# Optimization experiments

Measured on AMD Instinct MI355X. Metric: run time of the kernel, lower is better.

The kernel has to match this reference:

```python
import jax, jax.numpy as jnp
import numpy as np


def setup_inputs() -> dict:
    key = jax.random.key(0)
    ks = jax.random.split(key, 4)
    B, T, D, U = 32, 1024, 1024, 1024
    x = jax.random.normal(ks[0], (B, T, D), dtype=jnp.float32)
    W = jax.random.normal(ks[1], (D, 4 * U), dtype=jnp.float32) * (1.0 / np.sqrt(D))
    b = jnp.zeros((4 * U,), dtype=jnp.float32)
    Vr = jax.random.normal(ks[2], (U,), dtype=jnp.float32) * 0.1
    Vf = jax.random.normal(ks[3], (U,), dtype=jnp.float32) * 0.1
    h0 = jnp.zeros((B, U), dtype=jnp.float32)
    c0 = jnp.zeros((B, U), dtype=jnp.float32)
    return {"x": x, "h0": h0, "c0": c0, "W": W, "b": b, "Vr": Vr, "Vf": Vf}


def _sru(x, h0, c0, W, b, Vr, Vf):
    B, T, D = x.shape
    U = Vr.shape[0]
    # Batched matmul across all timesteps, then sequential elementwise scan.
    g = jnp.einsum('btd,dk->btk', x, W) + b            # [B, T, 4U]
    g = jnp.moveaxis(g, 1, 0)                          # [T, B, 4U]
    g1, g2, g3, g4 = jnp.split(g, 4, axis=-1)          # each [T, B, U]

    def step(c_, gs):
        a1, a2, a3, a4 = gs
        f = jax.nn.sigmoid(a1 + Vf * c_)
        c = f * c_ + (1.0 - f) * a2
        r = jax.nn.sigmoid(a3 + Vr * c_)
        h = r * c + (1.0 - r) * a4
        return c, h

    c_last, hs = jax.lax.scan(step, c0, (g1, g2, g3, g4))
    return jnp.moveaxis(hs, 0, 1)                      # [B, T, U]


def reference(x, h0, c0, W, b, Vr, Vf):
    return _sru(x, h0, c0, W, b, Vr, Vf)
```

## Files before the change

### kernel.cpp

```cpp
#include <hip/hip_runtime.h>
#include <cstdint>
#include <cstddef>

typedef short short8 __attribute__((ext_vector_type(8)));
typedef short s16x4 __attribute__((ext_vector_type(4)));
typedef float f32x4 __attribute__((ext_vector_type(4)));

typedef const __attribute__((address_space(1))) void* gas_ptr;
typedef __attribute__((address_space(3))) void* las_ptr;

__device__ __forceinline__ unsigned short f2bf(float f) {
    unsigned int u = __float_as_uint(f);
    u += 0x7fffu + ((u >> 16) & 1u);
    return (unsigned short)(u >> 16);
}
__device__ __forceinline__ float bf2f(unsigned short s) {
    return __uint_as_float(((unsigned int)s) << 16);
}
__device__ __forceinline__ float sigmoid_f(float z) {
    return __builtin_amdgcn_rcpf(1.0f + __expf(-z));
}
__device__ __forceinline__ void async_copy16(const void* gp, void* lp) {
    __builtin_amdgcn_global_load_lds((gas_ptr)gp, (las_ptr)lp, 16, 0, 0);
}

__global__ __launch_bounds__(256) void cvt_x_kernel(const float* __restrict__ in,
                                                    unsigned short* __restrict__ out) {
    size_t i = ((size_t)blockIdx.x * 256 + threadIdx.x) * 8;
    float4 v0 = *(const float4*)(in + i);
    float4 v1 = *(const float4*)(in + i + 4);
    short8 o;
    o[0]=(short)f2bf(v0.x); o[1]=(short)f2bf(v0.y); o[2]=(short)f2bf(v0.z); o[3]=(short)f2bf(v0.w);
    o[4]=(short)f2bf(v1.x); o[5]=(short)f2bf(v1.y); o[6]=(short)f2bf(v1.z); o[7]=(short)f2bf(v1.w);
    *(short8*)(out + i) = o;
}

__global__ __launch_bounds__(256) void cvt_w_kernel(const float* __restrict__ W,
                                                    unsigned short* __restrict__ Wt) {
    __shared__ unsigned short tile[64][65];
    int bk = blockIdx.x >> 6, bn = blockIdx.x & 63;
    int k0 = bk * 64, n0 = bn * 64;
    int t = threadIdx.x;
    int cr = t >> 6;
    int cc = t & 63;
#pragma unroll
    for (int i = 0; i < 16; ++i) {
        int row = i * 4 + cr;
        tile[row][cc] = f2bf(W[(size_t)(k0 + row) * 4096 + n0 + cc]);
    }
    __syncthreads();
#pragma unroll
    for (int i = 0; i < 16; ++i) {
        int nrow = i * 4 + cr;
        Wt[(size_t)(n0 + nrow) * 1024 + k0 + cc] = tile[cc][nrow];
    }
}

__global__ __launch_bounds__(256, 2) void gemm_kernel(const unsigned short* __restrict__ A,
                                                      const unsigned short* __restrict__ Bt,
                                                      const float* __restrict__ bias,
                                                      unsigned short* __restrict__ gT) {
    __shared__ __align__(16) unsigned short As[128 * 64];
    __shared__ __align__(16) unsigned short Bs[128 * 64];

    int bid = blockIdx.x;
    int band = bid >> 8;
    int r = bid & 255;
    int mt = band * 8 + (r >> 5);
    int nt = r & 31;
    int m0 = mt * 128, n0 = nt * 128;

    int tidx = threadIdx.x;
    int lane = tidx & 63, wv = tidx >> 6;
    int wm = wv >> 1, wn = wv & 1;
    int l15 = lane & 15, quad = lane >> 4;

    f32x4 acc[4][4] = {};

    for (int k0 = 0; k0 < 1024; k0 += 64) {
        __syncthreads();
#pragma unroll
        for (int i = 0; i < 4; ++i) {
            int ci = (wv * 4 + i) * 64 + lane;
            int row = ci >> 3, cc = ci & 7;
            int sc = (cc ^ (row & 7)) << 3;
            const unsigned short* ga = A + (size_t)(m0 + row) * 1024 + k0 + sc;
            async_copy16(ga, (char*)As + (wv * 4 + i) * 1024);
            const unsigned short* gb = Bt + (size_t)(n0 + row) * 1024 + k0 + sc;
            async_copy16(gb, (char*)Bs + (wv * 4 + i) * 1024);
        }
        __syncthreads();
#pragma unroll
        for (int kt = 0; kt < 2; ++kt) {
            short8 af[4], bf[4];
#pragma unroll
            for (int mt2 = 0; mt2 < 4; ++mt2) {
                int row = wm * 64 + mt2 * 16 + l15;
                int kc = kt * 4 + quad;
                af[mt2] = *(const short8*)((const char*)As + row * 128 + ((kc ^ (row & 7)) << 4));
            }
#pragma unroll
            for (int nt2 = 0; nt2 < 4; ++nt2) {
                int rown = wn * 64 + nt2 * 16 + l15;
                int kc = kt * 4 + quad;
                bf[nt2] = *(const short8*)((const char*)Bs + rown * 128 + ((kc ^ (rown & 7)) << 4));
            }
#pragma unroll
            for (int mt2 = 0; mt2 < 4; ++mt2)
#pragma unroll
                for (int nt2 = 0; nt2 < 4; ++nt2)
                    acc[mt2][nt2] = __builtin_amdgcn_mfma_f32_16x16x32_bf16(
                        af[mt2], bf[nt2], acc[mt2][nt2], 0, 0, 0);
        }
    }

#pragma unroll
    for (int mt2 = 0; mt2 < 4; ++mt2) {
        int mbase = m0 + wm * 64 + mt2 * 16 + quad * 4;
        int b_ = mbase >> 10, t_ = mbase & 1023;
#pragma unroll
        for (int nt2 = 0; nt2 < 4; ++nt2) {
            int n = n0 + wn * 64 + nt2 * 16 + l15;
            int gate = n >> 10, u = n & 1023;
            float bv = bias[n];
            s16x4 pk;
            pk[0] = (short)f2bf(acc[mt2][nt2][0] + bv);
            pk[1] = (short)f2bf(acc[mt2][nt2][1] + bv);
            pk[2] = (short)f2bf(acc[mt2][nt2][2] + bv);
            pk[3] = (short)f2bf(acc[mt2][nt2][3] + bv);
            size_t off = ((((size_t)(t_ >> 3) * 32 + (size_t)b_) * 4 + (size_t)gate) << 13)
                         + ((size_t)u << 3) + (size_t)(t_ & 7);
            *(s16x4*)(gT + off) = pk;
        }
    }
}

__global__ __launch_bounds__(128) void scan_c_kernel(const unsigned short* __restrict__ gT,
                                                     const float* __restrict__ c0,
                                                     const float* __restrict__ Vf,
                                                     float* __restrict__ cB) {
    __shared__ __align__(16) unsigned short sbuf[8 * 1024];

    const int NT = 112;
    const int D = 8;
    int blk = blockIdx.x;
    int b = blk >> 4;
    int u0 = (blk & 15) << 6;
    int tid = threadIdx.x;
    int wv = tid >> 6;
    int lane = tid & 63;

    if (wv == 0) {
        size_t base = ((size_t)b * 4) * 8192 + ((size_t)(u0 + lane) << 3);
        const unsigned short* pg0 = gT + base;
        const unsigned short* pg1 = pg0 + 8192;
#pragma unroll
        for (int g = 0; g < D - 1; ++g) {
            char* ld = (char*)sbuf + (g & 7) * 2048;
            size_t o = (size_t)g << 20;
            async_copy16(pg0 + o, ld);
            async_copy16(pg1 + o, ld + 1024);
        }
        for (int j = 0; j < NT; ++j) {
            if (j < NT - (D - 2)) {
                asm volatile("s_waitcnt vmcnt(12)" ::: "memory");
            } else {
                asm volatile("s_waitcnt vmcnt(0)" ::: "memory");
            }
            __builtin_amdgcn_s_barrier();
            int g = j + D - 1;
            if (g < NT) {
                char* ld = (char*)sbuf + (g & 7) * 2048;
                size_t o = (size_t)g << 20;
                async_copy16(pg0 + o, ld);
                async_copy16(pg1 + o, ld + 1024);
            }
        }
    } else {
        int u = u0 + lane;
        float c = c0[(b << 10) + u];
        float vf = Vf[u];
        const unsigned short* ls = sbuf + (size_t)lane * 8;
        for (int j = 0; j < NT; ++j) {
            __builtin_amdgcn_s_barrier();
            asm volatile("" ::: "memory");
            int so = (j & 7) * 1024;
            short8 a1 = *(const short8*)(ls + so);
            short8 a2 = *(const short8*)(ls + so + 512);
#pragma unroll
            for (int i = 0; i < 8; ++i) {
                float x1 = bf2f((unsigned short)a1[i]);
                float x2 = bf2f((unsigned short)a2[i]);
                float f  = sigmoid_f(x1 + vf * c);
                c = fmaf(f, c - x2, x2);
            }
            if ((j & 15) == 15) {
                cB[((size_t)(j >> 4) << 15) + (size_t)(b << 10) + u] = c;
            }
        }
    }
}

__global__ __launch_bounds__(256) void scan_h_kernel(const unsigned short* __restrict__ gT,
                                                     const float* __restrict__ c0,
                                                     const float* __restrict__ cB,
                                                     const float* __restrict__ Vr,
                                                     const float* __restrict__ Vf,
                                                     float* __restrict__ h) {
    int idx = blockIdx.x * 256 + threadIdx.x;
    int u = idx & 1023;
    int rb = idx >> 10;
    int r = rb >> 5, b = rb & 31;
    float vf = Vf[u], vr = Vr[u];
    float c = (r == 0) ? c0[(b << 10) + u]
                       : cB[((size_t)(r - 1) << 15) + (size_t)(b << 10) + u];
    const unsigned short* base = gT + ((size_t)b * 4) * 8192 + ((size_t)u << 3);
    float* hb = h + ((size_t)b << 20) + u;
    int tb0 = r << 4;

    const unsigned short* p0 = base + ((size_t)tb0 << 20);
    short8 n1 = *(const short8*)(p0);
    short8 n2 = *(const short8*)(p0 + 8192);
    short8 n3 = *(const short8*)(p0 + 16384);
    short8 n4 = *(const short8*)(p0 + 24576);
    for (int j = 0; j < 16; ++j) {
        short8 a1 = n1, a2 = n2, a3 = n3, a4 = n4;
        if (j < 15) {
            const unsigned short* q = base + ((size_t)(tb0 + j + 1) << 20);
            n1 = *(const short8*)(q);
            n2 = *(const short8*)(q + 8192);
            n3 = *(const short8*)(q + 16384);
            n4 = *(const short8*)(q + 24576);
        }
        int t0 = (tb0 + j) * 8;
#pragma unroll
        for (int i = 0; i < 8; ++i) {
            float x1 = bf2f((unsigned short)a1[i]);
            float x2 = bf2f((unsigned short)a2[i]);
            float x3 = bf2f((unsigned short)a3[i]);
            float x4 = bf2f((unsigned short)a4[i]);
            float f  = sigmoid_f(x1 + vf * c);
            float cp = c;
            c = fmaf(f, c - x2, x2);
            float rr = sigmoid_f(x3 + vr * cp);
            float hv = fmaf(rr, c - x4, x4);
            hb[(size_t)(t0 + i) << 10] = hv;
        }
    }
}

extern "C" void kernel_launch(void* const* d_in, const int* in_sizes, int n_in,
                              void* d_out, int out_size, void* d_ws, size_t ws_size,
                              hipStream_t stream) {
    const float* x  = (const float*)d_in[0];
    const float* c0 = (const float*)d_in[2];
    const float* W  = (const float*)d_in[3];
    const float* b  = (const float*)d_in[4];
    const float* Vr = (const float*)d_in[5];
    const float* Vf = (const float*)d_in[6];
    float* h = (float*)d_out;

    char* ws = (char*)d_ws;
    unsigned short* xb = (unsigned short*)ws;
    unsigned short* wt = (unsigned short*)(ws + (size_t)67108864);
    unsigned short* gT = (unsigned short*)(ws + (size_t)75497472);
    float* cB = (float*)ws;

    cvt_x_kernel<<<16384, 256, 0, stream>>>(x, xb);
    cvt_w_kernel<<<1024, 256, 0, stream>>>(W, wt);
    gemm_kernel<<<8192, 256, 0, stream>>>(xb, wt, b, gT);
    scan_c_kernel<<<512, 128, 0, stream>>>(gT, c0, Vf, cB);
    scan_h_kernel<<<1024, 256, 0, stream>>>(gT, c0, cB, Vr, Vf, h);
}
```

Measured before the change: 582.8 us.

## Rework scan_c to double-buffer 16-step chunks with seven loader waves

The scan_c kernel is restructured. Before, one loader wave fed a compute wave through an 8-slot ring with a barrier every 8 timesteps. Now seven loader waves fill a double-buffered 64KB LDS region holding 16 time blocks (128 steps) per chunk, and there is one __syncthreads per chunk. The goal is to cut per-step barrier and wait overhead and spread memory requests across more waves. In exchange, the first chunk load is fully exposed, the block uses much more LDS, and it runs 512 threads with only one wave doing compute.

```diff
diff --git a/kernel.cpp b/kernel.cpp
--- a/kernel.cpp
+++ b/kernel.cpp
@@ -135,14 +135,13 @@
     }
 }
 
-__global__ __launch_bounds__(128) void scan_c_kernel(const unsigned short* __restrict__ gT,
+__global__ __launch_bounds__(512) void scan_c_kernel(const unsigned short* __restrict__ gT,
                                                      const float* __restrict__ c0,
                                                      const float* __restrict__ Vf,
                                                      float* __restrict__ cB) {
-    __shared__ __align__(16) unsigned short sbuf[8 * 1024];
-
-    const int NT = 112;
-    const int D = 8;
+    __shared__ __align__(16) unsigned short sbuf[2 * 2 * 16 * 512];
+
+    const int NCH = 7;
     int blk = blockIdx.x;
     int b = blk >> 4;
     int u0 = (blk & 15) << 6;
@@ -150,54 +149,54 @@
     int wv = tid >> 6;
     int lane = tid & 63;
 
+    size_t gbase = (size_t)b * 32768 + ((size_t)(u0 + lane) << 3);
+
+    if (wv >= 1) {
+        for (int p = wv - 1; p < 32; p += 7) {
+            int gate = p >> 4, tbi = p & 15;
+            const unsigned short* src = gT + (((size_t)tbi) << 20) + gbase + gate * 8192;
+            char* dst = (char*)sbuf + gate * 16384 + tbi * 1024 + lane * 16;
+            async_copy16(src, dst);
+        }
+    }
+    __syncthreads();
+
+    float c = 0.0f, vf = 0.0f;
     if (wv == 0) {
-        size_t base = ((size_t)b * 4) * 8192 + ((size_t)(u0 + lane) << 3);
-        const unsigned short* pg0 = gT + base;
-        const unsigned short* pg1 = pg0 + 8192;
-#pragma unroll
-        for (int g = 0; g < D - 1; ++g) {
-            char* ld = (char*)sbuf + (g & 7) * 2048;
-            size_t o = (size_t)g << 20;
-            async_copy16(pg0 + o, ld);
-            async_copy16(pg1 + o, ld + 1024);
-        }
-        for (int j = 0; j < NT; ++j) {
-            if (j < NT - (D - 2)) {
-                asm volatile("s_waitcnt vmcnt(12)" ::: "memory");
-            } else {
-                asm volatile("s_waitcnt vmcnt(0)" ::: "memory");
-            }
-            __builtin_amdgcn_s_barrier();
-            int g = j + D - 1;
-            if (g < NT) {
-                char* ld = (char*)sbuf + (g & 7) * 2048;
-                size_t o = (size_t)g << 20;
-                async_copy16(pg0 + o, ld);
-                async_copy16(pg1 + o, ld + 1024);
-            }
-        }
-    } else {
         int u = u0 + lane;
-        float c = c0[(b << 10) + u];
-        float vf = Vf[u];
-        const unsigned short* ls = sbuf + (size_t)lane * 8;
-        for (int j = 0; j < NT; ++j) {
-            __builtin_amdgcn_s_barrier();
-            asm volatile("" ::: "memory");
-            int so = (j & 7) * 1024;
-            short8 a1 = *(const short8*)(ls + so);
-            short8 a2 = *(const short8*)(ls + so + 512);
-#pragma unroll
-            for (int i = 0; i < 8; ++i) {
-                float x1 = bf2f((unsigned short)a1[i]);
-                float x2 = bf2f((unsigned short)a2[i]);
-                float f  = sigmoid_f(x1 + vf * c);
-                c = fmaf(f, c - x2, x2);
-            }
-            if ((j & 15) == 15) {
-                cB[((size_t)(j >> 4) << 15) + (size_t)(b << 10) + u] = c;
-            }
-        }
+        c = c0[(b << 10) + u];
+        vf = Vf[u];
+    }
+
+    for (int k = 0; k < NCH; ++k) {
+        if (wv >= 1) {
+            if (k + 1 < NCH) {
+                int nb = (k + 1) & 1;
+                for (int p = wv - 1; p < 32; p += 7) {
+                    int gate = p >> 4, tbi = p & 15;
+                    const unsigned short* src =
+                        gT + (((size_t)((k + 1) * 16 + tbi)) << 20) + gbase + gate * 8192;
+                    char* dst = (char*)sbuf + nb * 32768 + gate * 16384 + tbi * 1024 + lane * 16;
+                    async_copy16(src, dst);
+                }
+            }
+        } else {
+            const unsigned short* ls = sbuf + (k & 1) * 16384 + (size_t)lane * 8;
+#pragma unroll
+            for (int tbi = 0; tbi < 16; ++tbi) {
+                short8 a1 = *(const short8*)(ls + tbi * 512);
+                short8 a2 = *(const short8*)(ls + 8192 + tbi * 512);
+#pragma unroll
+                for (int i = 0; i < 8; ++i) {
+                    float x1 = bf2f((unsigned short)a1[i]);
+                    float x2 = bf2f((unsigned short)a2[i]);
+                    float f  = sigmoid_f(x1 + vf * c);
+                    c = fmaf(f, c - x2, x2);
+                }
+            }
+            cB[((size_t)k << 15) + (size_t)(b << 10) + (size_t)(u0 + lane)] = c;
+        }
+        __syncthreads();
     }
 }
 
@@ -269,6 +268,6 @@
     cvt_x_kernel<<<16384, 256, 0, stream>>>(x, xb);
     cvt_w_kernel<<<1024, 256, 0, stream>>>(W, wt);
     gemm_kernel<<<8192, 256, 0, stream>>>(xb, wt, b, gT);
-    scan_c_kernel<<<512, 128, 0, stream>>>(gT, c0, Vf, cB);
+    scan_c_kernel<<<512, 512, 0, stream>>>(gT, c0, Vf, cB);
     scan_h_kernel<<<1024, 256, 0, stream>>>(gT, c0, cB, Vr, Vf, h);
 }
```

New measurement: 579.4 us. No clear change (-0.6%).
